# Performance work log

Hardware: AMD Instinct MI355X
Metric: run time of the kernel (lower is better)

## Reference

```python
import jax, jax.numpy as jnp
import numpy as np

B, K, H, W = 8, 32, 480, 480
N, D = 576, 1024
NUM_CLASSES, CLS_DIM, OUT = 150, 64, 256
IN_DIM = D + CLS_DIM + 5


def setup_inputs() -> dict:
    key = jax.random.key(0)
    ks = jax.random.split(key, 8)
    return {
        "feature_map": jax.random.normal(ks[0], (B, N, D), dtype=jnp.float32),
        "masks": jax.random.randint(ks[1], (B, K, H, W), 0, 2, dtype=jnp.int32),
        "class_ids": jax.random.randint(ks[2], (B, K), 0, NUM_CLASSES, dtype=jnp.int64),
        "embed_table": jax.random.normal(ks[3], (NUM_CLASSES, CLS_DIM), dtype=jnp.float32),
        "W1": jax.random.normal(ks[4], (IN_DIM, OUT), dtype=jnp.float32) * 0.02,
        "b1": jnp.zeros((OUT,), dtype=jnp.float32),
        "ln_g": jnp.ones((OUT,), dtype=jnp.float32),
        "ln_b": jnp.zeros((OUT,), dtype=jnp.float32),
        "W2": jax.random.normal(ks[5], (OUT, OUT), dtype=jnp.float32) * 0.02,
        "b2": jnp.zeros((OUT,), dtype=jnp.float32),
    }


def _geom_feats(m):
    # m: [B,K,H,W] float binary masks -> [B,K,5] (cx, cy, area_norm, bbox_w, bbox_h)
    dt = m.dtype
    area = m.sum((-2, -1))                      # [B,K]
    safe = jnp.maximum(area, 1.0)
    xs = jnp.arange(W, dtype=dt)
    ys = jnp.arange(H, dtype=dt)
    cx = jnp.einsum('bkhw,w->bk', m, xs) / safe / W
    cy = jnp.einsum('bkhw,h->bk', m, ys) / safe / H
    col = m.max(axis=2)                          # [B,K,W] column occupancy
    row = m.max(axis=3)                          # [B,K,H] row occupancy
    x_min = jnp.min(jnp.where(col > 0, xs, float(W)), axis=-1)
    x_max = jnp.max(jnp.where(col > 0, xs, -1.0), axis=-1)
    y_min = jnp.min(jnp.where(row > 0, ys, float(H)), axis=-1)
    y_max = jnp.max(jnp.where(row > 0, ys, -1.0), axis=-1)
    bbox_w = (x_max - x_min + 1.0) / W
    bbox_h = (y_max - y_min + 1.0) / H
    area_norm = area / (H * W)
    geom = jnp.stack([cx, cy, area_norm, bbox_w, bbox_h], axis=-1)  # [B,K,5]
    valid = (area >= 1.0)[..., None]
    return jnp.where(valid, geom, 0.0)


def reference(feature_map, masks, class_ids, embed_table, W1, b1, ln_g, ln_b, W2, b2):
    Hf = Wf = int(round(N ** 0.5))  # 24
    m = (masks > 0).astype(feature_map.dtype)           # [B,K,H,W]
    # nearest-neighbor downsample (PyTorch 'nearest': src = floor(dst*in/out))
    idx_h = (jnp.arange(Hf) * H) // Hf
    idx_w = (jnp.arange(Wf) * W) // Wf
    m_rs = m[:, :, idx_h][:, :, :, idx_w]               # [B,K,Hf,Wf]
    m_flat = m_rs.reshape(B, K, Hf * Wf)                # [B,K,N]
    msum = jnp.clip(m_flat.sum(-1, keepdims=True), 1e-6, None)
    pooled = jnp.einsum('bkn,bnd->bkd', m_flat, feature_map) / msum  # [B,K,D]
    geom = _geom_feats(m)                               # [B,K,5]
    cls_emb = embed_table[class_ids]                    # [B,K,CLS_DIM]
    x = jnp.concatenate([pooled, cls_emb, geom], axis=-1)  # [B,K,IN_DIM]
    h = jax.nn.gelu(x @ W1 + b1, approximate=False)
    mu = h.mean(-1, keepdims=True)
    var = jnp.mean((h - mu) ** 2, axis=-1, keepdims=True)
    hn = (h - mu) * jax.lax.rsqrt(var + 1e-5) * ln_g + ln_b
    return hn @ W2 + b2                                 # [B,K,OUT]
```

## Files before the change

### kernel.cpp

```cpp
#include <hip/hip_runtime.h>
#include <math.h>

#define Bb 8
#define Kk 32
#define Hh 480
#define Ww 480
#define Nn 576
#define Dd 1024
#define CLSD 64
#define OUTD 256
#define INDIM 1093
#define BK 256
#define PIX4 57600

__global__ __launch_bounds__(1024) void kF(const int* __restrict__ masks,
                                           const float* __restrict__ fm,
                                           const int* __restrict__ cids,
                                           const float* __restrict__ emb,
                                           const float* __restrict__ W1,
                                           const float* __restrict__ b1,
                                           const float* __restrict__ lg,
                                           const float* __restrict__ lb,
                                           const float* __restrict__ W2,
                                           const float* __restrict__ b2,
                                           float* __restrict__ out) {
  const int b    = blockIdx.x & 7;
  const int k    = blockIdx.x >> 3;
  const int bk   = b * Kk + k;
  const int t    = threadIdx.x;
  const int lane = t & 63;
  const int w    = t >> 6;

  __shared__ int    act[576];
  __shared__ float4 x4s[256];
  __shared__ float  partial[16 * 256];
  __shared__ float  hrow[256];
  __shared__ float  red_s[4], red_q[4];
  __shared__ float  gmeta[8];
  __shared__ int s_area, s_sumx, s_sumy;
  __shared__ int s_minx, s_maxx, s_miny, s_maxy, nact;

  if (t == 0) {
    s_area = 0; s_sumx = 0; s_sumy = 0;
    s_minx = Ww; s_maxx = -1; s_miny = Hh; s_maxy = -1;
    nact = 0;
  }
  __syncthreads();

  const int* mbase = masks + (size_t)bk * (Hh * Ww);
  if (t < 576) {
    int a = t / 24, c = t - a * 24;
    if (mbase[a * 20 * Ww + c * 20] > 0) act[atomicAdd(&nact, 1)] = t;
  }
  __syncthreads();
  const int na = nact;

  if (w < 12) {
    int area = 0, sumx = 0, sumy = 0;
    int minx = Ww, maxx = -1, miny = Hh, maxy = -1;
    const int4* mp = (const int4*)mbase;
#pragma unroll 5
    for (int i = 0; i < 75; i++) {
      int q = t + i * 768;
      int4 v = mp[q];
      int h   = q / 120;
      int rem = q - h * 120;
      int w0  = rem * 4;
      int m0 = v.x > 0, m1 = v.y > 0, m2 = v.z > 0, m3 = v.w > 0;
      int c = m0 + m1 + m2 + m3;
      area += c;
      sumy += h * c;
      sumx += w0 * c + m1 + 2 * m2 + 3 * m3;
      if (c) {
        miny = min(miny, h);
        maxy = max(maxy, h);
        int lo = m0 ? w0 : (m1 ? w0 + 1 : (m2 ? w0 + 2 : w0 + 3));
        int hi = m3 ? w0 + 3 : (m2 ? w0 + 2 : (m1 ? w0 + 1 : w0));
        minx = min(minx, lo);
        maxx = max(maxx, hi);
      }
    }
    for (int off = 32; off; off >>= 1) {
      area += __shfl_down(area, off);
      sumx += __shfl_down(sumx, off);
      sumy += __shfl_down(sumy, off);
      minx = min(minx, __shfl_down(minx, off));
      maxx = max(maxx, __shfl_down(maxx, off));
      miny = min(miny, __shfl_down(miny, off));
      maxy = max(maxy, __shfl_down(maxy, off));
    }
    if (lane == 0) {
      atomicAdd(&s_area, area);
      atomicAdd(&s_sumx, sumx);
      atomicAdd(&s_sumy, sumy);
      atomicMin(&s_minx, minx);
      atomicMax(&s_maxx, maxx);
      atomicMin(&s_miny, miny);
      atomicMax(&s_maxy, maxy);
    }
  } else {
    const int cw   = w - 12;
    const int base = cw * 64 + lane;
    const float4* fmp = (const float4*)fm + (size_t)b * Nn * (Dd / 4);
    float ax = 0.f, ay = 0.f, az = 0.f, aw = 0.f;
    int j = 0;
    for (; j + 4 <= na; j += 4) {
      int n0 = act[j], n1 = act[j + 1], n2 = act[j + 2], n3 = act[j + 3];
      float4 f0 = fmp[n0 * (Dd / 4) + base];
      float4 f1 = fmp[n1 * (Dd / 4) + base];
      float4 f2 = fmp[n2 * (Dd / 4) + base];
      float4 f3 = fmp[n3 * (Dd / 4) + base];
      ax += f0.x + f1.x + f2.x + f3.x;
      ay += f0.y + f1.y + f2.y + f3.y;
      az += f0.z + f1.z + f2.z + f3.z;
      aw += f0.w + f1.w + f2.w + f3.w;
    }
    for (; j < na; j++) {
      float4 f = fmp[act[j] * (Dd / 4) + base];
      ax += f.x; ay += f.y; az += f.z; aw += f.w;
    }
    float inv = 1.0f / fmaxf((float)na, 1e-6f);
    float4 xp;
    xp.x = ax * inv; xp.y = ay * inv; xp.z = az * inv; xp.w = aw * inv;
    x4s[base] = xp;

    float4 acc = {0.f, 0.f, 0.f, 0.f};
    const float* W1b = W1 + (size_t)(cw * 256) * OUTD + 4 * lane;
#pragma unroll 2
    for (int g = 0; g < 64; g++) {
      float4 xv = x4s[cw * 64 + g];
      const float* xs = (const float*)&xv;
#pragma unroll
      for (int u = 0; u < 4; u++) {
        float4 w4 = *(const float4*)(W1b + (size_t)(4 * g + u) * OUTD);
        acc.x = fmaf(xs[u], w4.x, acc.x);
        acc.y = fmaf(xs[u], w4.y, acc.y);
        acc.z = fmaf(xs[u], w4.z, acc.z);
        acc.w = fmaf(xs[u], w4.w, acc.w);
      }
    }
    *(float4*)(partial + cw * 256 + 4 * lane) = acc;
  }
  __syncthreads();

  if (t == 0) {
    float areaf = (float)s_area;
    float safe  = fmaxf(areaf, 1.0f);
    float cx = ((float)s_sumx / safe) * (1.0f / Ww);
    float cy = ((float)s_sumy / safe) * (1.0f / Hh);
    float an = areaf * (1.0f / (Hh * Ww));
    float bw = (float)(s_maxx - s_minx + 1) * (1.0f / Ww);
    float bh = (float)(s_maxy - s_miny + 1) * (1.0f / Hh);
    if (s_area < 1) { cx = 0.f; cy = 0.f; an = 0.f; bw = 0.f; bh = 0.f; }
    gmeta[0] = cx; gmeta[1] = cy; gmeta[2] = an; gmeta[3] = bw; gmeta[4] = bh;
  }
  __syncthreads();

  float hv = 0.f;
  if (t < 256) {
    hv = b1[t] + partial[t] + partial[256 + t] + partial[512 + t] + partial[768 + t];
    const float* et = emb + (size_t)cids[bk] * CLSD;
#pragma unroll 8
    for (int i = 0; i < CLSD; i++)
      hv = fmaf(et[i], W1[(size_t)(Dd + i) * OUTD + t], hv);
#pragma unroll
    for (int jj = 0; jj < 5; jj++)
      hv = fmaf(gmeta[jj], W1[(size_t)(Dd + CLSD + jj) * OUTD + t], hv);
    hv = 0.5f * hv * (1.0f + erff(hv * 0.7071067811865475f));
  }
  {
    float s = hv, q = hv * hv;
    for (int off = 32; off; off >>= 1) {
      s += __shfl_down(s, off);
      q += __shfl_down(q, off);
    }
    if (lane == 0 && w < 4) { red_s[w] = s; red_q[w] = q; }
  }
  __syncthreads();
  if (t < 256) {
    float s = red_s[0] + red_s[1] + red_s[2] + red_s[3];
    float q = red_q[0] + red_q[1] + red_q[2] + red_q[3];
    float mu  = s * (1.0f / OUTD);
    float var = q * (1.0f / OUTD) - mu * mu;
    float ist = 1.0f / sqrtf(var + 1e-5f);
    hrow[t] = (hv - mu) * ist * lg[t] + lb[t];
  }
  __syncthreads();

  {
    float4 acc = {0.f, 0.f, 0.f, 0.f};
#pragma unroll
    for (int i = 0; i < 4; i++) {
      float4 h4 = ((const float4*)hrow)[w * 4 + i];
      const float* hs = (const float*)&h4;
#pragma unroll
      for (int u = 0; u < 4; u++) {
        int kk = w * 16 + i * 4 + u;
        float4 w4 = *(const float4*)(W2 + (size_t)kk * OUTD + 4 * lane);
        acc.x = fmaf(hs[u], w4.x, acc.x);
        acc.y = fmaf(hs[u], w4.y, acc.y);
        acc.z = fmaf(hs[u], w4.z, acc.z);
        acc.w = fmaf(hs[u], w4.w, acc.w);
      }
    }
    *(float4*)(partial + w * 256 + 4 * lane) = acc;
  }
  __syncthreads();

  if (t < 256) {
    float c = b2[t];
#pragma unroll
    for (int ww = 0; ww < 16; ww++) c += partial[ww * 256 + t];
    out[(size_t)bk * OUTD + t] = c;
  }
}

extern "C" void kernel_launch(void* const* d_in, const int* in_sizes, int n_in,
                              void* d_out, int out_size, void* d_ws, size_t ws_size,
                              hipStream_t stream) {
  const float* fm    = (const float*)d_in[0];
  const int*   masks = (const int*)d_in[1];
  const int*   cids  = (const int*)d_in[2];
  const float* emb   = (const float*)d_in[3];
  const float* W1    = (const float*)d_in[4];
  const float* b1    = (const float*)d_in[5];
  const float* lg    = (const float*)d_in[6];
  const float* lb    = (const float*)d_in[7];
  const float* W2    = (const float*)d_in[8];
  const float* b2    = (const float*)d_in[9];
  float* out = (float*)d_out;

  hipLaunchKernelGGL(kF, dim3(BK), dim3(1024), 0, stream, masks, fm, cids, emb,
                     W1, b1, lg, lb, W2, b2, out);
}
```

Before: 372.1 us.

## Remove pre-phase barriers, use per-wave ballot compaction and nontemporal mask loads

New measurement: 370.0 us, median of 2. No clear change (-0.6%).

```diff
diff --git a/kernel.cpp b/kernel.cpp
--- a/kernel.cpp
+++ b/kernel.cpp
@@ -11,7 +11,8 @@
 #define OUTD 256
 #define INDIM 1093
 #define BK 256
-#define PIX4 57600
+
+typedef int v4i __attribute__((ext_vector_type(4)));
 
 __global__ __launch_bounds__(1024) void kF(const int* __restrict__ masks,
                                            const float* __restrict__ fm,
@@ -31,38 +32,24 @@
   const int lane = t & 63;
   const int w    = t >> 6;
 
-  __shared__ int    act[576];
+  __shared__ int    actw[4][576];
   __shared__ float4 x4s[256];
   __shared__ float  partial[16 * 256];
   __shared__ float  hrow[256];
   __shared__ float  red_s[4], red_q[4];
   __shared__ float  gmeta[8];
-  __shared__ int s_area, s_sumx, s_sumy;
-  __shared__ int s_minx, s_maxx, s_miny, s_maxy, nact;
-
-  if (t == 0) {
-    s_area = 0; s_sumx = 0; s_sumy = 0;
-    s_minx = Ww; s_maxx = -1; s_miny = Hh; s_maxy = -1;
-    nact = 0;
-  }
-  __syncthreads();
+  __shared__ int    gstat[12][7];
 
   const int* mbase = masks + (size_t)bk * (Hh * Ww);
-  if (t < 576) {
-    int a = t / 24, c = t - a * 24;
-    if (mbase[a * 20 * Ww + c * 20] > 0) act[atomicAdd(&nact, 1)] = t;
-  }
-  __syncthreads();
-  const int na = nact;
 
   if (w < 12) {
     int area = 0, sumx = 0, sumy = 0;
     int minx = Ww, maxx = -1, miny = Hh, maxy = -1;
-    const int4* mp = (const int4*)mbase;
+    const v4i* mp = (const v4i*)mbase;
 #pragma unroll 5
     for (int i = 0; i < 75; i++) {
       int q = t + i * 768;
-      int4 v = mp[q];
+      v4i v = __builtin_nontemporal_load(mp + q);
       int h   = q / 120;
       int rem = q - h * 120;
       int w0  = rem * 4;
@@ -90,22 +77,36 @@
       maxy = max(maxy, __shfl_down(maxy, off));
     }
     if (lane == 0) {
-      atomicAdd(&s_area, area);
-      atomicAdd(&s_sumx, sumx);
-      atomicAdd(&s_sumy, sumy);
-      atomicMin(&s_minx, minx);
-      atomicMax(&s_maxx, maxx);
-      atomicMin(&s_miny, miny);
-      atomicMax(&s_maxy, maxy);
+      gstat[w][0] = area; gstat[w][1] = sumx; gstat[w][2] = sumy;
+      gstat[w][3] = minx; gstat[w][4] = maxx;
+      gstat[w][5] = miny; gstat[w][6] = maxy;
     }
   } else {
     const int cw   = w - 12;
     const int base = cw * 64 + lane;
+
+    int mv[9];
+#pragma unroll
+    for (int r = 0; r < 9; r++) {
+      int p = r * 64 + lane;
+      int a = p / 24, c = p - a * 24;
+      mv[r] = mbase[(a * 20) * Ww + c * 20];
+    }
+    int na = 0;
+    int* actp = actw[cw];
+#pragma unroll
+    for (int r = 0; r < 9; r++) {
+      unsigned long long bal = __ballot(mv[r] > 0);
+      int idx = __popcll(bal & ((1ull << lane) - 1));
+      if (mv[r] > 0) actp[na + idx] = r * 64 + lane;
+      na += __popcll(bal);
+    }
+
     const float4* fmp = (const float4*)fm + (size_t)b * Nn * (Dd / 4);
     float ax = 0.f, ay = 0.f, az = 0.f, aw = 0.f;
     int j = 0;
     for (; j + 4 <= na; j += 4) {
-      int n0 = act[j], n1 = act[j + 1], n2 = act[j + 2], n3 = act[j + 3];
+      int n0 = actp[j], n1 = actp[j + 1], n2 = actp[j + 2], n3 = actp[j + 3];
       float4 f0 = fmp[n0 * (Dd / 4) + base];
       float4 f1 = fmp[n1 * (Dd / 4) + base];
       float4 f2 = fmp[n2 * (Dd / 4) + base];
@@ -116,7 +117,7 @@
       aw += f0.w + f1.w + f2.w + f3.w;
     }
     for (; j < na; j++) {
-      float4 f = fmp[act[j] * (Dd / 4) + base];
+      float4 f = fmp[actp[j] * (Dd / 4) + base];
       ax += f.x; ay += f.y; az += f.z; aw += f.w;
     }
     float inv = 1.0f / fmaxf((float)na, 1e-6f);
@@ -144,14 +145,22 @@
   __syncthreads();
 
   if (t == 0) {
-    float areaf = (float)s_area;
+    int area = 0, sumx = 0, sumy = 0;
+    int minx = Ww, maxx = -1, miny = Hh, maxy = -1;
+#pragma unroll
+    for (int i = 0; i < 12; i++) {
+      area += gstat[i][0]; sumx += gstat[i][1]; sumy += gstat[i][2];
+      minx = min(minx, gstat[i][3]); maxx = max(maxx, gstat[i][4]);
+      miny = min(miny, gstat[i][5]); maxy = max(maxy, gstat[i][6]);
+    }
+    float areaf = (float)area;
     float safe  = fmaxf(areaf, 1.0f);
-    float cx = ((float)s_sumx / safe) * (1.0f / Ww);
-    float cy = ((float)s_sumy / safe) * (1.0f / Hh);
+    float cx = ((float)sumx / safe) * (1.0f / Ww);
+    float cy = ((float)sumy / safe) * (1.0f / Hh);
     float an = areaf * (1.0f / (Hh * Ww));
-    float bw = (float)(s_maxx - s_minx + 1) * (1.0f / Ww);
-    float bh = (float)(s_maxy - s_miny + 1) * (1.0f / Hh);
-    if (s_area < 1) { cx = 0.f; cy = 0.f; an = 0.f; bw = 0.f; bh = 0.f; }
+    float bw = (float)(maxx - minx + 1) * (1.0f / Ww);
+    float bh = (float)(maxy - miny + 1) * (1.0f / Hh);
+    if (area < 1) { cx = 0.f; cy = 0.f; an = 0.f; bw = 0.f; bh = 0.f; }
     gmeta[0] = cx; gmeta[1] = cy; gmeta[2] = an; gmeta[3] = bw; gmeta[4] = bh;
   }
   __syncthreads();
@@ -211,7 +220,7 @@
     float c = b2[t];
 #pragma unroll
     for (int ww = 0; ww < 16; ww++) c += partial[ww * 256 + t];
-    out[(size_t)bk * OUTD + t] = c;
+    __builtin_nontemporal_store(c, out + (size_t)bk * OUTD + t);
   }
 }
 
```
